# Kernel optimization log

Hardware: AMD Instinct MI355X
Metric: run time of the kernel (lower is better)

The kernel has to match this reference:

```python
import jax, jax.numpy as jnp
import numpy as np

N_NODES = 30000
N_EDGES = 600000
N_BATCH = 8
VFRAMES = 3
EPS = 1e-20


def rbf_func(D, num_rbf=16):
    # RBF over [0, 20] with num_rbf centers, matching torch rbf_func
    mu = jnp.linspace(0.0, 20.0, num_rbf).astype(D.dtype)
    sigma = 20.0 / num_rbf
    return jnp.exp(-(((D[..., None] - mu) / sigma) ** 2))


def decouple(U):
    # split vector into unit direction (zeroed when tiny) + RBF of its norm -> last dim 3+16
    sq = jnp.sum(U * U, axis=-1, keepdims=True)
    norm = jnp.sqrt(sq + 1e-12)  # tiny eps for grad safety; fwd diff negligible
    direct = jnp.where(norm < 1e-4, 0.0, U / (norm + 1e-6))
    return jnp.concatenate([direct, rbf_func(norm[..., 0])], axis=-1)


def int_embedding(d, num_embeddings):
    freq = jnp.exp(jnp.arange(0, num_embeddings, 2, dtype=jnp.float32) * (-np.log(10000.0) / num_embeddings))
    ang = d.astype(jnp.float32)[:, None] * freq[None, :]
    return jnp.concatenate([jnp.cos(ang), jnp.sin(ang)], axis=-1)


def make_frames(n_xyz, ca_xyz, c_xyz):
    # openfold Rigid.make_transform_from_reference -> R [N,3,3], t = CA [N,3]
    n = n_xyz - ca_xyz
    c = c_xyz - ca_xyz
    cx, cy, cz = c[:, 0], c[:, 1], c[:, 2]
    z = jnp.zeros_like(cx)
    o = jnp.ones_like(cx)
    nrm = jnp.sqrt(EPS + cx ** 2 + cy ** 2)
    s1, c1 = -cy / nrm, cx / nrm
    R1 = jnp.stack([c1, -s1, z, s1, c1, z, z, z, o], -1).reshape(-1, 3, 3)
    nrm2 = jnp.sqrt(EPS + cx ** 2 + cy ** 2 + cz ** 2)
    s2 = cz / nrm2
    c2 = jnp.sqrt(cx ** 2 + cy ** 2) / nrm2
    R2 = jnp.stack([c2, z, s2, z, o, z, -s2, z, c2], -1).reshape(-1, 3, 3)
    Rc = jnp.matmul(R2, R1)
    nrot = jnp.einsum('nij,nj->ni', Rc, n)
    ny, nz2 = nrot[:, 1], nrot[:, 2]
    nrm3 = jnp.sqrt(EPS + ny ** 2 + nz2 ** 2)
    sn, cn = -nz2 / nrm3, ny / nrm3
    Rn = jnp.stack([o, z, z, z, cn, -sn, z, sn, cn], -1).reshape(-1, 3, 3)
    R = jnp.swapaxes(jnp.matmul(Rn, Rc), -1, -2)
    return R, ca_xyz


def geo_features(X, node_idx, edge_idx, batch_id, num_batches, virtual_frame_num):
    N = X.shape[0]
    E = edge_idx.shape[1]
    B = num_batches          # static python int
    K = virtual_frame_num    # static python int
    src, dst = edge_idx[0], edge_idx[1]
    R, t = make_frames(X[:, 0], X[:, 1], X[:, 2])
    # relative transform T_ts = T[dst]^-1 . T[src]
    Rts = jnp.einsum('eji,ejk->eik', R[dst], R[src])            # [E,3,3]
    tts = jnp.einsum('eji,ej->ei', R[dst], t[src] - t[dst])     # [E,3]
    # node feats: consecutive-atom diffs, zeroed at each chain start, rotated into local frame
    flat = X.reshape(-1, 3)
    d = jnp.concatenate([jnp.zeros((1, 3), X.dtype), flat[1:] - flat[:-1]], 0).reshape(N, 4, 3)
    counts = jax.ops.segment_sum(jnp.ones_like(batch_id), batch_id, num_segments=B)
    shift = jnp.roll(jnp.cumsum(counts).at[-1].set(0), 1)       # chain start offsets
    d = d.at[shift].set(0.0)
    dX_loc = jnp.einsum('nji,naj->nai', R, d)                   # R^T @ d
    V = jnp.nan_to_num(decouple(dX_loc).reshape(N, -1))         # [N,76]
    # edge feats: both endpoints' atoms in src local frame
    pts = jnp.concatenate([X[src], X[dst]], axis=1)             # [E,8,3]
    loc = jnp.einsum('eji,eaj->eai', R[src], pts - t[src][:, None])
    diffE = decouple(loc).reshape(E, -1)                        # [E,152]
    pos = int_embedding((src - dst), 16)                        # [E,16]
    E_quant = jnp.swapaxes(Rts, -1, -2).reshape(E, 9)           # inverse rel-rot flattened
    E_trans = decouple(tts).reshape(E, -1)                      # [E,19]
    b = (node_idx[src] - node_idx[dst]).astype(X.dtype)
    E_bias = decouple(b[:, None, None]).reshape(E, -1)          # [E,17]
    Efeat = jnp.concatenate([diffE, E_quant, E_trans, pos, E_bias], axis=-1)  # [E,213]
    # virtual (global) frames: K virtual nodes per protein, identity frames (geo_frame=False)
    g_src = jnp.concatenate([N + batch_id + k * B for k in range(K)])   # [K*N]
    g_dst = jnp.tile(jnp.arange(N, dtype=batch_id.dtype), K)
    eidx_g = jnp.concatenate([jnp.stack([g_src, g_dst]), jnp.stack([g_dst, g_src])], axis=1)
    bid_g = jnp.tile(jnp.arange(B, dtype=batch_id.dtype), K)            # [K*B]
    V_g = int_embedding(jnp.repeat(jnp.arange(K), B), V.shape[-1]).astype(X.dtype)
    E_g = jnp.zeros((2 * K * N, Efeat.shape[-1]), Efeat.dtype)
    eyeKB = jnp.broadcast_to(jnp.eye(3, dtype=X.dtype), (K * B, 3, 3))
    V_out = jnp.concatenate([V, V_g], 0)
    E_out = jnp.concatenate([Efeat, E_g], 0)
    T_rot = jnp.concatenate([R, eyeKB], 0)
    T_trans = jnp.concatenate([t, jnp.zeros((K * B, 3), X.dtype)], 0)
    Tts_rot = jnp.concatenate([Rts, jnp.broadcast_to(jnp.eye(3, dtype=X.dtype), (2 * K * N, 3, 3))], 0)
    Tts_trans = jnp.concatenate([tts, jnp.zeros((2 * K * N, 3), X.dtype)], 0)
    batch_out = jnp.concatenate([batch_id, bid_g])
    eidx_out = jnp.concatenate([edge_idx, eidx_g], axis=1)
    return V_out, E_out, T_rot, T_trans, Tts_rot, Tts_trans, batch_out, eidx_out


def setup_inputs():
    key = jax.random.key(0)
    k1, k2 = jax.random.split(key)
    X = jax.random.normal(k1, (N_NODES, 4, 3), dtype=jnp.float32) * 4.0
    edge_idx = jax.random.randint(k2, (2, N_EDGES), 0, N_NODES)
    per = N_NODES // N_BATCH
    batch_id = jnp.repeat(jnp.arange(N_BATCH), per)   # sorted, contiguous batches
    node_idx = jnp.tile(jnp.arange(per), N_BATCH)     # residue index within each chain
    chain_encoding = batch_id % 8
    return {"X": X, "node_idx": node_idx, "edge_idx": edge_idx, "batch_id": batch_id,
            "chain_encoding": chain_encoding, "num_batches": N_BATCH, "virtual_frame_num": VFRAMES}


def reference(X, node_idx, edge_idx, batch_id, chain_encoding, num_batches, virtual_frame_num):
    V, Eo, T_rot, T_trans, Tts_rot, Tts_trans, batch_out, eidx_out = geo_features(
        X, node_idx, edge_idx, batch_id, num_batches, virtual_frame_num)
    K, B = virtual_frame_num, num_batches
    chain_out = jnp.concatenate([chain_encoding,
                                 jnp.ones((K * B,), chain_encoding.dtype) + 1000])
    return (V, Eo, T_rot, T_trans, Tts_rot, Tts_trans, batch_out, eidx_out, chain_out)
```

## Files before the change

### kernel.cpp

```cpp
#include <hip/hip_runtime.h>

typedef unsigned int u32;

#define N_NODES 30000
#define N_EDGES 600000
#define NBATCH  8
#define KVF     3
#define PER_B   3750
#define NV      30024
#define EV      780000

#define O_V      0ULL
#define O_E      2281824ULL
#define O_TROT   168421824ULL
#define O_TTRANS 168692040ULL
#define O_TTSROT 168782112ULL
#define O_TTSTR  175802112ULL
#define O_BATCH  178142112ULL
#define O_EIDX   178172136ULL
#define O_CHAIN  179732136ULL

__device__ __forceinline__ void decouple_store(float u0, float u1, float u2, float* dst) {
    float sq   = u0 * u0 + u1 * u1 + u2 * u2;
    float norm = sqrtf(sq + 1e-12f);
    float inv  = (norm < 1e-4f) ? 0.f : (1.f / (norm + 1e-6f));
    dst[0] = u0 * inv;
    dst[1] = u1 * inv;
    dst[2] = u2 * inv;
#pragma unroll
    for (int k = 0; k < 16; ++k) {
        float mu = 1.3333333333333333f * (float)k;
        float z  = (norm - mu) * 0.8f;
        dst[3 + k] = __expf(-z * z);
    }
}

__global__ __launch_bounds__(256) void node_kernel(
        const float* __restrict__ X, const int* __restrict__ batch_id,
        const int* __restrict__ chain, float* __restrict__ out,
        float* __restrict__ rec) {
    int i = blockIdx.x * blockDim.x + threadIdx.x;
    if (i >= NV) return;
    if (i < N_NODES) {
        const float* xi = X + (size_t)i * 12;
        float cax = xi[3], cay = xi[4], caz = xi[5];
        float nx = xi[0] - cax, ny = xi[1] - cay, nz = xi[2] - caz;
        float cx = xi[6] - cax, cy = xi[7] - cay, cz = xi[8] - caz;
        float h2   = cx * cx + cy * cy;
        float nrm  = sqrtf(1e-20f + h2);
        float s1 = -cy / nrm, c1 = cx / nrm;
        float nrm2 = sqrtf(1e-20f + h2 + cz * cz);
        float s2 = cz / nrm2, c2 = sqrtf(h2) / nrm2;
        float Rc00 = c2 * c1, Rc01 = -c2 * s1, Rc02 = s2;
        float Rc10 = s1,      Rc11 = c1;
        float Rc20 = -s2 * c1, Rc21 = s2 * s1, Rc22 = c2;
        float nr1 = Rc10 * nx + Rc11 * ny;
        float nr2 = Rc20 * nx + Rc21 * ny + Rc22 * nz;
        float nrm3 = sqrtf(1e-20f + nr1 * nr1 + nr2 * nr2);
        float sn = -nr2 / nrm3, cn = nr1 / nrm3;
        float M00 = Rc00, M01 = Rc01, M02 = Rc02;
        float M10 = cn * Rc10 - sn * Rc20, M11 = cn * Rc11 - sn * Rc21, M12 = -sn * Rc22;
        float M20 = sn * Rc10 + cn * Rc20, M21 = sn * Rc11 + cn * Rc21, M22 = cn * Rc22;
        float r0 = M00, r1 = M10, r2 = M20;
        float r3 = M01, r4 = M11, r5 = M21;
        float r6 = M02, r7 = M12, r8 = M22;
        float* rw = rec + (size_t)i * 12;
        rw[0] = r0; rw[1] = r1; rw[2] = r2; rw[3] = r3; rw[4] = r4;
        rw[5] = r5; rw[6] = r6; rw[7] = r7; rw[8] = r8;
        rw[9] = cax; rw[10] = cay; rw[11] = caz;
        float* tr = out + O_TROT + (size_t)i * 9;
        tr[0] = r0; tr[1] = r1; tr[2] = r2;
        tr[3] = r3; tr[4] = r4; tr[5] = r5;
        tr[6] = r6; tr[7] = r7; tr[8] = r8;
        float* tt = out + O_TTRANS + (size_t)i * 3;
        tt[0] = cax; tt[1] = cay; tt[2] = caz;
        float* vp = out + O_V + (size_t)i * 76;
        bool zero_d = (i % PER_B) == 0;
#pragma unroll
        for (int a = 0; a < 4; ++a) {
            float d0, d1, d2;
            if (zero_d) {
                d0 = d1 = d2 = 0.f;
            } else {
                const float* pc = xi + a * 3;
                d0 = pc[0] - pc[-3]; d1 = pc[1] - pc[-2]; d2 = pc[2] - pc[-1];
            }
            float u0 = M00 * d0 + M01 * d1 + M02 * d2;
            float u1 = M10 * d0 + M11 * d1 + M12 * d2;
            float u2 = M20 * d0 + M21 * d1 + M22 * d2;
            decouple_store(u0, u1, u2, vp + a * 19);
        }
        out[O_BATCH + i] = (float)batch_id[i];
        out[O_CHAIN + i] = (float)chain[i];
    } else {
        int r = i - N_NODES;
        float kv = (float)(r >> 3);
        float* vp = out + O_V + (size_t)i * 76;
#pragma unroll
        for (int j = 0; j < 38; ++j) {
            float freq = __expf((float)(2 * j) * (-9.210340371976184f / 76.f));
            float ang  = kv * freq;
            vp[j]      = cosf(ang);
            vp[38 + j] = sinf(ang);
        }
        float* tr = out + O_TROT + (size_t)i * 9;
#pragma unroll
        for (int j = 0; j < 9; ++j) tr[j] = (j == 0 || j == 4 || j == 8) ? 1.f : 0.f;
        float* tt = out + O_TTRANS + (size_t)i * 3;
        tt[0] = 0.f; tt[1] = 0.f; tt[2] = 0.f;
        out[O_BATCH + i] = (float)(r & 7);
        out[O_CHAIN + i] = 1001.f;
    }
}

__global__ __launch_bounds__(256) void edge_kernel(
        const float* __restrict__ X, const int* __restrict__ eidx,
        const int* __restrict__ node_idx, const float* __restrict__ rec,
        float* __restrict__ out) {
    __shared__ __align__(16) float sE[64 * 213];
    __shared__ __align__(16) float sRot[64 * 9];
    __shared__ __align__(16) float sTr[64 * 3];
    int tid  = threadIdx.x;
    int el   = tid & 63;
    int part = tid >> 6;
    int e = blockIdx.x * 64 + el;
    int src = eidx[e];
    int dst = eidx[N_EDGES + e];
    float* se = sE + el * 213;

    if (part <= 1) {
        const float4* rs4 = (const float4*)(rec + (size_t)src * 12);
        float4 rA = rs4[0], rB = rs4[1], rC = rs4[2];
        float ts0 = rC.y, ts1 = rC.z, ts2 = rC.w;
        int nd = (part == 0) ? src : dst;
        const float4* xv = (const float4*)(X + (size_t)nd * 12);
        float4 x0 = xv[0], x1 = xv[1], x2 = xv[2];
        float px[4] = { x0.x, x0.w, x1.z, x2.y };
        float py[4] = { x0.y, x1.x, x1.w, x2.z };
        float pz[4] = { x0.z, x1.y, x2.x, x2.w };
        float* base = se + (part == 0 ? 0 : 76);
#pragma unroll
        for (int a = 0; a < 4; ++a) {
            float p0 = px[a] - ts0, p1 = py[a] - ts1, p2 = pz[a] - ts2;
            float u0 = rA.x * p0 + rA.w * p1 + rB.z * p2;
            float u1 = rA.y * p0 + rB.x * p1 + rB.w * p2;
            float u2 = rA.z * p0 + rB.y * p1 + rC.x * p2;
            decouple_store(u0, u1, u2, base + a * 19);
        }
    } else if (part == 2) {
        const float4* rs4 = (const float4*)(rec + (size_t)src * 12);
        float4 sA = rs4[0], sB = rs4[1], sC = rs4[2];
        const float4* rd4 = (const float4*)(rec + (size_t)dst * 12);
        float4 dA = rd4[0], dB = rd4[1], dC = rd4[2];
        float Rs[9] = { sA.x, sA.y, sA.z, sA.w, sB.x, sB.y, sB.z, sB.w, sC.x };
        float Rd[9] = { dA.x, dA.y, dA.z, dA.w, dB.x, dB.y, dB.z, dB.w, dC.x };
        float ts0 = sC.y, ts1 = sC.z, ts2 = sC.w;
        float td0 = dC.y, td1 = dC.z, td2 = dC.w;
        float* sr = sRot + el * 9;
#pragma unroll
        for (int ii = 0; ii < 3; ++ii) {
#pragma unroll
            for (int k = 0; k < 3; ++k) {
                float q = Rd[ii] * Rs[k] + Rd[3 + ii] * Rs[3 + k] + Rd[6 + ii] * Rs[6 + k];
                sr[ii * 3 + k] = q;
                se[152 + k * 3 + ii] = q;
            }
        }
        float dt0 = ts0 - td0, dt1 = ts1 - td1, dt2 = ts2 - td2;
        float t0 = Rd[0] * dt0 + Rd[3] * dt1 + Rd[6] * dt2;
        float t1 = Rd[1] * dt0 + Rd[4] * dt1 + Rd[7] * dt2;
        float t2 = Rd[2] * dt0 + Rd[5] * dt1 + Rd[8] * dt2;
        float* st = sTr + el * 3;
        st[0] = t0; st[1] = t1; st[2] = t2;
        decouple_store(t0, t1, t2, se + 161);
    } else {
        float dd = (float)(src - dst);
#pragma unroll
        for (int j = 0; j < 8; ++j) {
            float freq = __expf((float)(2 * j) * (-9.210340371976184f / 16.f));
            float ang  = dd * freq;
            se[180 + j] = cosf(ang);
            se[188 + j] = sinf(ang);
        }
        float b    = (float)(node_idx[src] - node_idx[dst]);
        float norm = sqrtf(b * b + 1e-12f);
        se[196] = (norm < 1e-4f) ? 0.f : (b / (norm + 1e-6f));
#pragma unroll
        for (int k = 0; k < 16; ++k) {
            float z = (norm - 1.3333333333333333f * (float)k) * 0.8f;
            se[197 + k] = __expf(-z * z);
        }
    }
    __syncthreads();
    const uint4* s4 = (const uint4*)sE;
    uint4* dE = (uint4*)(out + O_E) + (size_t)blockIdx.x * 3408;
    for (int i2 = tid; i2 < 3408; i2 += 256) dE[i2] = s4[i2];
    if (tid < 144) ((uint4*)(out + O_TTSROT))[(size_t)blockIdx.x * 144 + tid] = ((const uint4*)sRot)[tid];
    if (tid < 48)  ((uint4*)(out + O_TTSTR))[(size_t)blockIdx.x * 48 + tid]   = ((const uint4*)sTr)[tid];
}

__global__ void fill_ve(float* __restrict__ out) {
    size_t i = (size_t)blockIdx.x * blockDim.x + threadIdx.x;
    if (i < 9585000ULL) {
        uint4 z; z.x = z.y = z.z = z.w = 0u;
        ((uint4*)(out + O_E + 600000ULL * 213ULL))[i] = z;
    }
}

__global__ void fill_tts(float* __restrict__ out) {
    int i = blockIdx.x * blockDim.x + threadIdx.x;
    if (i < 1620000) {
        int a = i % 9;
        out[O_TTSROT + 5400000ULL + i] = (a == 0 || a == 4 || a == 8) ? 1.f : 0.f;
    }
    if (i < 135000) {
        uint4 z; z.x = z.y = z.z = z.w = 0u;
        ((uint4*)(out + O_TTSTR + 1800000ULL))[i] = z;
    }
}

__global__ void eidx_kernel(const int* __restrict__ ei, const int* __restrict__ batch_id,
                            float* __restrict__ out) {
    int i = blockIdx.x * blockDim.x + threadIdx.x;
    if (i >= 2 * EV) return;
    int row = i / EV;
    int col = i - row * EV;
    int v;
    if (col < N_EDGES) {
        v = ei[row * N_EDGES + col];
    } else {
        int j    = col - N_EDGES;
        int half = j / 90000;
        int jj   = j - half * 90000;
        int k    = jj / N_NODES;
        int node = jj - k * N_NODES;
        bool takeSrc = (row == 0) ? (half == 0) : (half == 1);
        v = takeSrc ? (N_NODES + batch_id[node] + k * NBATCH) : node;
    }
    out[O_EIDX + i] = (float)v;
}

extern "C" void kernel_launch(void* const* d_in, const int* in_sizes, int n_in,
                              void* d_out, int out_size, void* d_ws, size_t ws_size,
                              hipStream_t stream) {
    const float* X        = (const float*)d_in[0];
    const int* node_idx   = (const int*)d_in[1];
    const int* eidx       = (const int*)d_in[2];
    const int* batch_id   = (const int*)d_in[3];
    const int* chain      = (const int*)d_in[4];
    float* out = (float*)d_out;
    float* rec = (float*)d_ws;

    node_kernel<<<(NV + 255) / 256, 256, 0, stream>>>(X, batch_id, chain, out, rec);
    edge_kernel<<<N_EDGES / 64, 256, 0, stream>>>(X, eidx, node_idx, rec, out);
    fill_ve<<<(9585000 + 255) / 256, 256, 0, stream>>>(out);
    fill_tts<<<(1620000 + 255) / 256, 256, 0, stream>>>(out);
    eidx_kernel<<<(2 * EV + 255) / 256, 256, 0, stream>>>(eidx, batch_id, out);
}
```

Baseline: 750.8 us.

## Fuse all stages into one kernel, recompute frames per edge, nontemporal stores

Replaces the five separate launches with a single kernel. Every fourth block does node work, or else grid-strided fill of the virtual-edge region, the Tts fill and eidx output, while the other blocks process edges. The per-node frame record in the workspace is gone: edge threads recompute the src/dst frames from X, which adds ALU work but removes the node-to-edge dependency and the extra launches. All large outputs are written with nontemporal vector stores to reduce cache pollution on the write-dominated workload.

```diff
diff --git a/kernel.cpp b/kernel.cpp
--- a/kernel.cpp
+++ b/kernel.cpp
@@ -1,6 +1,7 @@
 #include <hip/hip_runtime.h>
 
 typedef unsigned int u32;
+typedef float f32x4 __attribute__((ext_vector_type(4)));
 
 #define N_NODES 30000
 #define N_EDGES 600000
@@ -20,6 +21,14 @@
 #define O_EIDX   178172136ULL
 #define O_CHAIN  179732136ULL
 
+#define TOTAL_BLOCKS 12500
+#define NODE_BLOCKS  118
+#define FILL_THREADS 769792ULL
+#define F_VE   9585000ULL
+#define F_ROT  (F_VE + 405000ULL)
+#define F_TR   (F_ROT + 135000ULL)
+#define F_END  (F_TR + 390000ULL)
+
 __device__ __forceinline__ void decouple_store(float u0, float u1, float u2, float* dst) {
     float sq   = u0 * u0 + u1 * u1 + u2 * u2;
     float norm = sqrtf(sq + 1e-12f);
@@ -35,141 +44,199 @@
     }
 }
 
-__global__ __launch_bounds__(256) void node_kernel(
-        const float* __restrict__ X, const int* __restrict__ batch_id,
-        const int* __restrict__ chain, float* __restrict__ out,
-        float* __restrict__ rec) {
-    int i = blockIdx.x * blockDim.x + threadIdx.x;
-    if (i >= NV) return;
-    if (i < N_NODES) {
-        const float* xi = X + (size_t)i * 12;
-        float cax = xi[3], cay = xi[4], caz = xi[5];
-        float nx = xi[0] - cax, ny = xi[1] - cay, nz = xi[2] - caz;
-        float cx = xi[6] - cax, cy = xi[7] - cay, cz = xi[8] - caz;
-        float h2   = cx * cx + cy * cy;
-        float nrm  = sqrtf(1e-20f + h2);
-        float s1 = -cy / nrm, c1 = cx / nrm;
-        float nrm2 = sqrtf(1e-20f + h2 + cz * cz);
-        float s2 = cz / nrm2, c2 = sqrtf(h2) / nrm2;
-        float Rc00 = c2 * c1, Rc01 = -c2 * s1, Rc02 = s2;
-        float Rc10 = s1,      Rc11 = c1;
-        float Rc20 = -s2 * c1, Rc21 = s2 * s1, Rc22 = c2;
-        float nr1 = Rc10 * nx + Rc11 * ny;
-        float nr2 = Rc20 * nx + Rc21 * ny + Rc22 * nz;
-        float nrm3 = sqrtf(1e-20f + nr1 * nr1 + nr2 * nr2);
-        float sn = -nr2 / nrm3, cn = nr1 / nrm3;
-        float M00 = Rc00, M01 = Rc01, M02 = Rc02;
-        float M10 = cn * Rc10 - sn * Rc20, M11 = cn * Rc11 - sn * Rc21, M12 = -sn * Rc22;
-        float M20 = sn * Rc10 + cn * Rc20, M21 = sn * Rc11 + cn * Rc21, M22 = cn * Rc22;
-        float r0 = M00, r1 = M10, r2 = M20;
-        float r3 = M01, r4 = M11, r5 = M21;
-        float r6 = M02, r7 = M12, r8 = M22;
-        float* rw = rec + (size_t)i * 12;
-        rw[0] = r0; rw[1] = r1; rw[2] = r2; rw[3] = r3; rw[4] = r4;
-        rw[5] = r5; rw[6] = r6; rw[7] = r7; rw[8] = r8;
-        rw[9] = cax; rw[10] = cay; rw[11] = caz;
-        float* tr = out + O_TROT + (size_t)i * 9;
-        tr[0] = r0; tr[1] = r1; tr[2] = r2;
-        tr[3] = r3; tr[4] = r4; tr[5] = r5;
-        tr[6] = r6; tr[7] = r7; tr[8] = r8;
-        float* tt = out + O_TTRANS + (size_t)i * 3;
-        tt[0] = cax; tt[1] = cay; tt[2] = caz;
-        float* vp = out + O_V + (size_t)i * 76;
-        bool zero_d = (i % PER_B) == 0;
-#pragma unroll
-        for (int a = 0; a < 4; ++a) {
-            float d0, d1, d2;
-            if (zero_d) {
-                d0 = d1 = d2 = 0.f;
-            } else {
-                const float* pc = xi + a * 3;
-                d0 = pc[0] - pc[-3]; d1 = pc[1] - pc[-2]; d2 = pc[2] - pc[-1];
-            }
-            float u0 = M00 * d0 + M01 * d1 + M02 * d2;
-            float u1 = M10 * d0 + M11 * d1 + M12 * d2;
-            float u2 = M20 * d0 + M21 * d1 + M22 * d2;
-            decouple_store(u0, u1, u2, vp + a * 19);
-        }
-        out[O_BATCH + i] = (float)batch_id[i];
-        out[O_CHAIN + i] = (float)chain[i];
-    } else {
-        int r = i - N_NODES;
-        float kv = (float)(r >> 3);
-        float* vp = out + O_V + (size_t)i * 76;
-#pragma unroll
-        for (int j = 0; j < 38; ++j) {
-            float freq = __expf((float)(2 * j) * (-9.210340371976184f / 76.f));
-            float ang  = kv * freq;
-            vp[j]      = cosf(ang);
-            vp[38 + j] = sinf(ang);
-        }
-        float* tr = out + O_TROT + (size_t)i * 9;
-#pragma unroll
-        for (int j = 0; j < 9; ++j) tr[j] = (j == 0 || j == 4 || j == 8) ? 1.f : 0.f;
-        float* tt = out + O_TTRANS + (size_t)i * 3;
-        tt[0] = 0.f; tt[1] = 0.f; tt[2] = 0.f;
-        out[O_BATCH + i] = (float)(r & 7);
-        out[O_CHAIN + i] = 1001.f;
-    }
-}
-
-__global__ __launch_bounds__(256) void edge_kernel(
+__device__ __forceinline__ void make_frame(float4 x0, float4 x1, float4 x2,
+                                           float M[9], float& t0, float& t1, float& t2) {
+    float cax = x0.w, cay = x1.x, caz = x1.y;
+    float nx = x0.x - cax, ny = x0.y - cay, nz = x0.z - caz;
+    float cx = x1.z - cax, cy = x1.w - cay, cz = x2.x - caz;
+    float h2   = cx * cx + cy * cy;
+    float nrm  = sqrtf(1e-20f + h2);
+    float s1 = -cy / nrm, c1 = cx / nrm;
+    float nrm2 = sqrtf(1e-20f + h2 + cz * cz);
+    float s2 = cz / nrm2, c2 = sqrtf(h2) / nrm2;
+    float Rc00 = c2 * c1, Rc01 = -c2 * s1, Rc02 = s2;
+    float Rc10 = s1,      Rc11 = c1;
+    float Rc20 = -s2 * c1, Rc21 = s2 * s1, Rc22 = c2;
+    float nr1 = Rc10 * nx + Rc11 * ny;
+    float nr2 = Rc20 * nx + Rc21 * ny + Rc22 * nz;
+    float nrm3 = sqrtf(1e-20f + nr1 * nr1 + nr2 * nr2);
+    float sn = -nr2 / nrm3, cn = nr1 / nrm3;
+    M[0] = Rc00;                   M[1] = Rc01;                   M[2] = Rc02;
+    M[3] = cn * Rc10 - sn * Rc20;  M[4] = cn * Rc11 - sn * Rc21;  M[5] = -sn * Rc22;
+    M[6] = sn * Rc10 + cn * Rc20;  M[7] = sn * Rc11 + cn * Rc21;  M[8] = cn * Rc22;
+    t0 = cax; t1 = cay; t2 = caz;
+}
+
+__global__ __launch_bounds__(256) void mega_kernel(
         const float* __restrict__ X, const int* __restrict__ eidx,
-        const int* __restrict__ node_idx, const float* __restrict__ rec,
-        float* __restrict__ out) {
+        const int* __restrict__ node_idx, const int* __restrict__ batch_id,
+        const int* __restrict__ chain, float* __restrict__ out) {
     __shared__ __align__(16) float sE[64 * 213];
     __shared__ __align__(16) float sRot[64 * 9];
     __shared__ __align__(16) float sTr[64 * 3];
-    int tid  = threadIdx.x;
+
+    int bid = blockIdx.x;
+    int tid = threadIdx.x;
+
+    if ((bid & 3) == 3) {
+        int oblk = bid >> 2;
+        if (oblk < NODE_BLOCKS) {
+            int i = oblk * 256 + tid;
+            if (i >= NV) return;
+            if (i < N_NODES) {
+                const float4* xv = (const float4*)(X + (size_t)i * 12);
+                float4 x0 = xv[0], x1 = xv[1], x2 = xv[2];
+                float M[9], cax, cay, caz;
+                make_frame(x0, x1, x2, M, cax, cay, caz);
+                float* tr = out + O_TROT + (size_t)i * 9;
+                tr[0] = M[0]; tr[1] = M[3]; tr[2] = M[6];
+                tr[3] = M[1]; tr[4] = M[4]; tr[5] = M[7];
+                tr[6] = M[2]; tr[7] = M[5]; tr[8] = M[8];
+                float* tt = out + O_TTRANS + (size_t)i * 3;
+                tt[0] = cax; tt[1] = cay; tt[2] = caz;
+                const float* xi = X + (size_t)i * 12;
+                float* vp = out + O_V + (size_t)i * 76;
+                bool zero_d = (i % PER_B) == 0;
+#pragma unroll
+                for (int a = 0; a < 4; ++a) {
+                    float d0, d1, d2;
+                    if (zero_d) {
+                        d0 = d1 = d2 = 0.f;
+                    } else {
+                        const float* pc = xi + a * 3;
+                        d0 = pc[0] - pc[-3]; d1 = pc[1] - pc[-2]; d2 = pc[2] - pc[-1];
+                    }
+                    float u0 = M[0] * d0 + M[1] * d1 + M[2] * d2;
+                    float u1 = M[3] * d0 + M[4] * d1 + M[5] * d2;
+                    float u2 = M[6] * d0 + M[7] * d1 + M[8] * d2;
+                    decouple_store(u0, u1, u2, vp + a * 19);
+                }
+                out[O_BATCH + i] = (float)batch_id[i];
+                out[O_CHAIN + i] = (float)chain[i];
+            } else {
+                int r = i - N_NODES;
+                float kv = (float)(r >> 3);
+                float* vp = out + O_V + (size_t)i * 76;
+#pragma unroll
+                for (int j = 0; j < 38; ++j) {
+                    float freq = __expf((float)(2 * j) * (-9.210340371976184f / 76.f));
+                    float ang  = kv * freq;
+                    vp[j]      = cosf(ang);
+                    vp[38 + j] = sinf(ang);
+                }
+                float* tr = out + O_TROT + (size_t)i * 9;
+#pragma unroll
+                for (int j = 0; j < 9; ++j) tr[j] = (j == 0 || j == 4 || j == 8) ? 1.f : 0.f;
+                float* tt = out + O_TTRANS + (size_t)i * 3;
+                tt[0] = 0.f; tt[1] = 0.f; tt[2] = 0.f;
+                out[O_BATCH + i] = (float)(r & 7);
+                out[O_CHAIN + i] = 1001.f;
+            }
+            return;
+        }
+        f32x4* oE   = (f32x4*)(out + O_E + 600000ULL * 213ULL);
+        f32x4* oRot = (f32x4*)(out + O_TTSROT + 5400000ULL);
+        f32x4* oTr  = (f32x4*)(out + O_TTSTR + 1800000ULL);
+        f32x4* oEi  = (f32x4*)(out + O_EIDX);
+        f32x4 zero; zero.x = zero.y = zero.z = zero.w = 0.f;
+        for (size_t f = (size_t)(oblk - NODE_BLOCKS) * 256 + tid; f < F_END; f += FILL_THREADS) {
+            if (f < F_VE) {
+                __builtin_nontemporal_store(zero, oE + f);
+            } else if (f < F_ROT) {
+                size_t f2 = f - F_VE;
+                u32 a = (u32)((f2 * 4ULL) % 9ULL);
+                f32x4 w;
+#pragma unroll
+                for (int l = 0; l < 4; ++l) {
+                    w[l] = (a == 0u || a == 4u || a == 8u) ? 1.f : 0.f;
+                    a = (a == 8u) ? 0u : a + 1u;
+                }
+                __builtin_nontemporal_store(w, oRot + f2);
+            } else if (f < F_TR) {
+                __builtin_nontemporal_store(zero, oTr + (f - F_ROT));
+            } else {
+                size_t f4 = f - F_TR;
+                int i0 = (int)(f4 * 4);
+                f32x4 w;
+#pragma unroll
+                for (int l = 0; l < 4; ++l) {
+                    int i = i0 + l;
+                    int row = (i >= EV) ? 1 : 0;
+                    int col = i - row * EV;
+                    float v;
+                    if (col < N_EDGES) {
+                        v = (float)eidx[row * N_EDGES + col];
+                    } else {
+                        int j    = col - N_EDGES;
+                        int half = j / 90000;
+                        int jj   = j - half * 90000;
+                        int k    = jj / N_NODES;
+                        int node = jj - k * N_NODES;
+                        v = (row == half) ? (float)(N_NODES + batch_id[node] + k * NBATCH)
+                                          : (float)node;
+                    }
+                    w[l] = v;
+                }
+                __builtin_nontemporal_store(w, oEi + f4);
+            }
+        }
+        return;
+    }
+
+    int eblk = (bid >> 2) * 3 + (bid & 3);
     int el   = tid & 63;
     int part = tid >> 6;
-    int e = blockIdx.x * 64 + el;
+    int e = eblk * 64 + el;
     int src = eidx[e];
     int dst = eidx[N_EDGES + e];
     float* se = sE + el * 213;
 
     if (part <= 1) {
-        const float4* rs4 = (const float4*)(rec + (size_t)src * 12);
-        float4 rA = rs4[0], rB = rs4[1], rC = rs4[2];
-        float ts0 = rC.y, ts1 = rC.z, ts2 = rC.w;
-        int nd = (part == 0) ? src : dst;
-        const float4* xv = (const float4*)(X + (size_t)nd * 12);
-        float4 x0 = xv[0], x1 = xv[1], x2 = xv[2];
-        float px[4] = { x0.x, x0.w, x1.z, x2.y };
-        float py[4] = { x0.y, x1.x, x1.w, x2.z };
-        float pz[4] = { x0.z, x1.y, x2.x, x2.w };
+        const float4* xs = (const float4*)(X + (size_t)src * 12);
+        float4 s0 = xs[0], s1 = xs[1], s2 = xs[2];
+        float4 p0 = s0, p1 = s1, p2 = s2;
+        if (part == 1) {
+            const float4* xd = (const float4*)(X + (size_t)dst * 12);
+            p0 = xd[0]; p1 = xd[1]; p2 = xd[2];
+        }
+        float M[9], ts0, ts1, ts2;
+        make_frame(s0, s1, s2, M, ts0, ts1, ts2);
+        float px[4] = { p0.x, p0.w, p1.z, p2.y };
+        float py[4] = { p0.y, p1.x, p1.w, p2.z };
+        float pz[4] = { p0.z, p1.y, p2.x, p2.w };
         float* base = se + (part == 0 ? 0 : 76);
 #pragma unroll
         for (int a = 0; a < 4; ++a) {
-            float p0 = px[a] - ts0, p1 = py[a] - ts1, p2 = pz[a] - ts2;
-            float u0 = rA.x * p0 + rA.w * p1 + rB.z * p2;
-            float u1 = rA.y * p0 + rB.x * p1 + rB.w * p2;
-            float u2 = rA.z * p0 + rB.y * p1 + rC.x * p2;
+            float q0 = px[a] - ts0, q1 = py[a] - ts1, q2 = pz[a] - ts2;
+            float u0 = M[0] * q0 + M[1] * q1 + M[2] * q2;
+            float u1 = M[3] * q0 + M[4] * q1 + M[5] * q2;
+            float u2 = M[6] * q0 + M[7] * q1 + M[8] * q2;
             decouple_store(u0, u1, u2, base + a * 19);
         }
     } else if (part == 2) {
-        const float4* rs4 = (const float4*)(rec + (size_t)src * 12);
-        float4 sA = rs4[0], sB = rs4[1], sC = rs4[2];
-        const float4* rd4 = (const float4*)(rec + (size_t)dst * 12);
-        float4 dA = rd4[0], dB = rd4[1], dC = rd4[2];
-        float Rs[9] = { sA.x, sA.y, sA.z, sA.w, sB.x, sB.y, sB.z, sB.w, sC.x };
-        float Rd[9] = { dA.x, dA.y, dA.z, dA.w, dB.x, dB.y, dB.z, dB.w, dC.x };
-        float ts0 = sC.y, ts1 = sC.z, ts2 = sC.w;
-        float td0 = dC.y, td1 = dC.z, td2 = dC.w;
+        const float4* xs = (const float4*)(X + (size_t)src * 12);
+        const float4* xd = (const float4*)(X + (size_t)dst * 12);
+        float4 s0 = xs[0], s1 = xs[1], s2 = xs[2];
+        float4 d0 = xd[0], d1 = xd[1], d2 = xd[2];
+        float Ms[9], ts0, ts1, ts2;
+        float Md[9], td0, td1, td2;
+        make_frame(s0, s1, s2, Ms, ts0, ts1, ts2);
+        make_frame(d0, d1, d2, Md, td0, td1, td2);
         float* sr = sRot + el * 9;
 #pragma unroll
         for (int ii = 0; ii < 3; ++ii) {
 #pragma unroll
             for (int k = 0; k < 3; ++k) {
-                float q = Rd[ii] * Rs[k] + Rd[3 + ii] * Rs[3 + k] + Rd[6 + ii] * Rs[6 + k];
+                float q = Md[3 * ii] * Ms[3 * k] + Md[3 * ii + 1] * Ms[3 * k + 1]
+                        + Md[3 * ii + 2] * Ms[3 * k + 2];
                 sr[ii * 3 + k] = q;
                 se[152 + k * 3 + ii] = q;
             }
         }
         float dt0 = ts0 - td0, dt1 = ts1 - td1, dt2 = ts2 - td2;
-        float t0 = Rd[0] * dt0 + Rd[3] * dt1 + Rd[6] * dt2;
-        float t1 = Rd[1] * dt0 + Rd[4] * dt1 + Rd[7] * dt2;
-        float t2 = Rd[2] * dt0 + Rd[5] * dt1 + Rd[8] * dt2;
+        float t0 = Md[0] * dt0 + Md[1] * dt1 + Md[2] * dt2;
+        float t1 = Md[3] * dt0 + Md[4] * dt1 + Md[5] * dt2;
+        float t2 = Md[6] * dt0 + Md[7] * dt1 + Md[8] * dt2;
         float* st = sTr + el * 3;
         st[0] = t0; st[1] = t1; st[2] = t2;
         decouple_store(t0, t1, t2, se + 161);
@@ -192,52 +259,16 @@
         }
     }
     __syncthreads();
-    const uint4* s4 = (const uint4*)sE;
-    uint4* dE = (uint4*)(out + O_E) + (size_t)blockIdx.x * 3408;
-    for (int i2 = tid; i2 < 3408; i2 += 256) dE[i2] = s4[i2];
-    if (tid < 144) ((uint4*)(out + O_TTSROT))[(size_t)blockIdx.x * 144 + tid] = ((const uint4*)sRot)[tid];
-    if (tid < 48)  ((uint4*)(out + O_TTSTR))[(size_t)blockIdx.x * 48 + tid]   = ((const uint4*)sTr)[tid];
-}
-
-__global__ void fill_ve(float* __restrict__ out) {
-    size_t i = (size_t)blockIdx.x * blockDim.x + threadIdx.x;
-    if (i < 9585000ULL) {
-        uint4 z; z.x = z.y = z.z = z.w = 0u;
-        ((uint4*)(out + O_E + 600000ULL * 213ULL))[i] = z;
-    }
-}
-
-__global__ void fill_tts(float* __restrict__ out) {
-    int i = blockIdx.x * blockDim.x + threadIdx.x;
-    if (i < 1620000) {
-        int a = i % 9;
-        out[O_TTSROT + 5400000ULL + i] = (a == 0 || a == 4 || a == 8) ? 1.f : 0.f;
-    }
-    if (i < 135000) {
-        uint4 z; z.x = z.y = z.z = z.w = 0u;
-        ((uint4*)(out + O_TTSTR + 1800000ULL))[i] = z;
-    }
-}
-
-__global__ void eidx_kernel(const int* __restrict__ ei, const int* __restrict__ batch_id,
-                            float* __restrict__ out) {
-    int i = blockIdx.x * blockDim.x + threadIdx.x;
-    if (i >= 2 * EV) return;
-    int row = i / EV;
-    int col = i - row * EV;
-    int v;
-    if (col < N_EDGES) {
-        v = ei[row * N_EDGES + col];
-    } else {
-        int j    = col - N_EDGES;
-        int half = j / 90000;
-        int jj   = j - half * 90000;
-        int k    = jj / N_NODES;
-        int node = jj - k * N_NODES;
-        bool takeSrc = (row == 0) ? (half == 0) : (half == 1);
-        v = takeSrc ? (N_NODES + batch_id[node] + k * NBATCH) : node;
-    }
-    out[O_EIDX + i] = (float)v;
+    const f32x4* s4 = (const f32x4*)sE;
+    f32x4* dE = (f32x4*)(out + O_E) + (size_t)eblk * 3408;
+    for (int i2 = tid; i2 < 3408; i2 += 256)
+        __builtin_nontemporal_store(s4[i2], dE + i2);
+    if (tid < 144)
+        __builtin_nontemporal_store(((const f32x4*)sRot)[tid],
+                                    (f32x4*)(out + O_TTSROT) + (size_t)eblk * 144 + tid);
+    if (tid < 48)
+        __builtin_nontemporal_store(((const f32x4*)sTr)[tid],
+                                    (f32x4*)(out + O_TTSTR) + (size_t)eblk * 48 + tid);
 }
 
 extern "C" void kernel_launch(void* const* d_in, const int* in_sizes, int n_in,
@@ -249,11 +280,7 @@
     const int* batch_id   = (const int*)d_in[3];
     const int* chain      = (const int*)d_in[4];
     float* out = (float*)d_out;
-    float* rec = (float*)d_ws;
-
-    node_kernel<<<(NV + 255) / 256, 256, 0, stream>>>(X, batch_id, chain, out, rec);
-    edge_kernel<<<N_EDGES / 64, 256, 0, stream>>>(X, eidx, node_idx, rec, out);
-    fill_ve<<<(9585000 + 255) / 256, 256, 0, stream>>>(out);
-    fill_tts<<<(1620000 + 255) / 256, 256, 0, stream>>>(out);
-    eidx_kernel<<<(2 * EV + 255) / 256, 256, 0, stream>>>(eidx, batch_id, out);
-}
+    (void)d_ws; (void)ws_size;
+
+    mega_kernel<<<TOTAL_BLOCKS, 256, 0, stream>>>(X, eidx, node_idx, batch_id, chain, out);
+}
```

New measurement: 714.1 us. 4.9% less time.
